# Performance work log

Measured on AMD Instinct MI355X. Metric: run time of the kernel, lower is better.

The kernel has to match this reference:

```python
import jax, jax.numpy as jnp
import numpy as np

L, S, R, NUM_RESNET = 6, 2, 3, 3
N = 2 ** L            # 64 blocks per axis
NX = N * S            # 128 grid points per axis
NCART_SIDE = 80
NCART = NCART_SIDE ** 2


def _perm_idx(L_, l):
    delta = 2 ** (L_ - l - 1)
    t = np.tile(np.arange(2) * delta, delta) + np.repeat(np.arange(delta), 2)
    t = np.tile(t, 2 ** l) + np.repeat(np.arange(2 ** l) * 2 ** (L_ - l), 2 ** (L_ - l))
    return jnp.asarray(t)


def _switch_idx(L_):
    h = L_ // 2
    t = np.tile(np.arange(2 ** h) * 2 ** h, 2 ** h) + np.repeat(np.arange(2 ** h), 2 ** h)
    return jnp.asarray(t)


def _bmm2(x, g_left, g_right):
    # x: (B,p,i,q,j). Right block-diag GEMM on (q,j), then left block-diag GEMM on (p,i).
    y = jnp.einsum('bpiqj,qjk->bpiqk', x, g_right)
    return jnp.einsum('bpiqk,pio->bpoqk', y, g_left)


def _complex_layer(xr, xi, p):
    # p: stacked (r1,i1,r2,i2,r3,i3,r4,i4); complex-style cross products of the original.
    r1, i1, r2, i2, r3, i3, r4, i4 = p
    yr = _bmm2(xr, r1, r1) + _bmm2(xr, i1, i1) + _bmm2(xi, r2, i2) + _bmm2(xi, i2, r2)
    yi = _bmm2(xi, r3, r3) + _bmm2(xi, i3, i3) + _bmm2(xr, r4, i4) + _bmm2(xr, i4, r4)
    return yr, yi


def _u_layer(xr, xi, p):
    ur1, ui1, ur2, ui2, ur3, ui3, ur4, ui4 = p
    return (_bmm2(xr, ur1, ur1) + _bmm2(xr, ui2, ui2)
            + _bmm2(xi, ur3, ui3) + _bmm2(xi, ui4, ur4))


def _permute(yr, yi, idx):
    yr = jnp.take(jnp.take(yr, idx, axis=1), idx, axis=3)
    yi = jnp.take(jnp.take(yi, idx, axis=1), idx, axis=3)
    return yr, yi


def _merge(y):  # (B,N,R,N,R) -> (B,N/2,2R,N/2,2R)
    return y.reshape(y.shape[0], N // 2, 2 * R, N // 2, 2 * R)


def _split(y):  # inverse of _merge
    return y.reshape(y.shape[0], N, R, N, R)


def reference(x, Vp, Hp, Mp, Gp, Up, cart_mat, r_index):
    B = x.shape[0]
    xr = x[..., 0].reshape(B, N, S, N, S)
    xi = x[..., 1].reshape(B, N, S, N, S)
    yr, yi = _complex_layer(xr, xi, Vp)                       # (B,N,R,N,R)
    for li, l in enumerate(range(L - 1, L // 2 - 1, -1)):     # H stages (permute then merge-GEMM)
        yr, yi = _permute(yr, yi, _perm_idx(L, l))
        yr, yi = _complex_layer(_merge(yr), _merge(yi), Hp[li])
        yr, yi = _split(yr), _split(yi)
    yr, yi = _permute(yr, yi, _switch_idx(L))                 # middle switch shuffle
    for k in range(NUM_RESNET):                               # residual M blocks
        zr, zi = _complex_layer(yr, yi, Mp[k])
        yr, yi = yr + zr, yi + zi
    for li, l in enumerate(range(L // 2 - 1, -1, -1)):        # G stages (merge-GEMM then permute)
        yr, yi = _complex_layer(_merge(yr), _merge(yi), Gp[li])
        yr, yi = _split(yr), _split(yi)
        yr, yi = _permute(yr, yi, _perm_idx(L, l))
    y = _u_layer(yr, yi, Up).reshape(B, NX * NX)              # real output, (B,NX,NX) flattened
    y = jnp.take(y, r_index, axis=1)                          # polar reindexing
    out = y @ cart_mat.T                                      # polar -> cartesian interpolation
    return out.reshape(B, NCART_SIDE, NCART_SIDE)


def setup_inputs() -> dict:
    key = jax.random.key(0)
    ks = jax.random.split(key, 9)
    B = 128
    x = jax.random.normal(ks[0], (B, NX, NX, 2), dtype=jnp.float32)
    Vp = jax.random.normal(ks[1], (8, N, S, R), dtype=jnp.float32) * 0.35
    Hp = jax.random.normal(ks[2], (L // 2, 8, N // 2, 2 * R, 2 * R), dtype=jnp.float32) * 0.2
    Mp = jax.random.normal(ks[3], (NUM_RESNET, 8, N, R, R), dtype=jnp.float32) * 0.25
    Gp = jax.random.normal(ks[4], (L // 2, 8, N // 2, 2 * R, 2 * R), dtype=jnp.float32) * 0.2
    Up = jax.random.normal(ks[5], (8, N, R, S), dtype=jnp.float32) * 0.35
    cart_mat = jax.random.normal(ks[6], (NCART, NX * NX), dtype=jnp.float32) * 0.01
    r_index = jax.random.permutation(ks[7], NX * NX).astype(jnp.int32)
    return {"x": x, "Vp": Vp, "Hp": Hp, "Mp": Mp, "Gp": Gp, "Up": Up,
            "cart_mat": cart_mat, "r_index": r_index}
```

## Files before the change

### kernel.cpp

```cpp
#include <hip/hip_runtime.h>


typedef _Float16 f16;
typedef __attribute__((ext_vector_type(8))) short sx8;
typedef __attribute__((ext_vector_type(4))) float fx4;
typedef __attribute__((ext_vector_type(8))) unsigned short usx8;
typedef __attribute__((ext_vector_type(4))) unsigned short usx4;

__device__ __forceinline__ unsigned short f2bf(float f) {
  unsigned u = __builtin_bit_cast(unsigned, f);
  u = (u + 0x7FFFu + ((u >> 16) & 1u)) >> 16;
  return (unsigned short)u;
}
__device__ __forceinline__ float bf2f(unsigned short h) {
  return __builtin_bit_cast(float, ((unsigned)h) << 16);
}

template<int ID>
__device__ __forceinline__ int rp_apply(int k) {
  if constexpr (ID == 0) { return k; }
  else if constexpr (ID == 3) { return (k & 7) * 8 + (k >> 3); }
  else {
    constexpr int l = (ID == 1) ? 4 : (ID == 2) ? 3 : (ID == 4) ? 2 : (ID == 5) ? 1 : 0;
    constexpr int d = 1 << (5 - l);
    constexpr int m2 = 2 * d;
    int g = k / m2, r = k % m2;
    return g * m2 + (r & 1) * d + (r >> 1);
  }
}

__global__ __launch_bounds__(256) void k_transpose(const float* __restrict__ x,
                                                   f16* __restrict__ xtr,
                                                   f16* __restrict__ xti) {
  __shared__ float ls[2][32][129];
  const int t = threadIdx.x;
  const int u = blockIdx.x;
  const int v0 = blockIdx.y * 32;
  for (int it = 0; it < 32; ++it) {
    int b = it * 4 + (t >> 6);
    int r = t & 63;
    int v = r >> 1, ch = r & 1;
    ls[ch][v][b] = x[(((size_t)b * 128 + u) * 128 + (v0 + v)) * 2 + ch];
  }
  __syncthreads();
  for (int it = 0; it < 32; ++it) {
    int idx = it * 256 + t;
    int ch = idx >> 12;
    int v = (idx >> 7) & 31;
    int b = idx & 127;
    f16* dst = ch ? xti : xtr;
    dst[((size_t)(u * 128 + v0 + v)) * 128 + b] = (f16)ls[ch][v][b];
  }
}

__global__ __launch_bounds__(128, 1) void k_vh(const f16* __restrict__ xtr,
                                               const f16* __restrict__ xti,
                                               f16* __restrict__ yr,
                                               f16* __restrict__ yi,
                                               const float* __restrict__ vp,
                                               const float* __restrict__ hp) {
  const int b = threadIdx.x;
  const int P = blockIdx.x, Q = blockIdx.y;
  float Vr[36], Vi[36];

#pragma unroll
  for (int pp = 0; pp < 2; ++pp)
#pragma unroll
    for (int qq = 0; qq < 2; ++qq) {
      const int p = 2 * P + pp, q = 2 * Q + qq;
      float Xr[4], Xi[4];
#pragma unroll
      for (int i = 0; i < 2; ++i)
#pragma unroll
        for (int j = 0; j < 2; ++j) {
          size_t off = ((size_t)((4 * P + 2 * pp + i) * 128 + (4 * Q + 2 * qq + j))) * 128 + b;
          Xr[i * 2 + j] = (float)xtr[off];
          Xi[i * 2 + j] = (float)xti[off];
        }
      float Ar[9], Ai[9];
#pragma unroll
      for (int k = 0; k < 9; ++k) { Ar[k] = 0.f; Ai[k] = 0.f; }
      auto termV = [&](float* Y, const float* X, int lm, int rm) {
        const float* Lw = vp + ((size_t)lm * 64 + p) * 6;
        const float* Rw = vp + ((size_t)rm * 64 + q) * 6;
#pragma unroll
        for (int i = 0; i < 2; ++i) {
          float t0 = X[i*2+0] * Rw[0] + X[i*2+1] * Rw[3];
          float t1 = X[i*2+0] * Rw[1] + X[i*2+1] * Rw[4];
          float t2 = X[i*2+0] * Rw[2] + X[i*2+1] * Rw[5];
#pragma unroll
          for (int o = 0; o < 3; ++o) {
            float lv = Lw[i * 3 + o];
            Y[o*3+0] += lv * t0; Y[o*3+1] += lv * t1; Y[o*3+2] += lv * t2;
          }
        }
      };
      termV(Ar, Xr, 0, 0); termV(Ar, Xr, 1, 1); termV(Ai, Xr, 6, 7); termV(Ai, Xr, 7, 6);
      termV(Ar, Xi, 2, 3); termV(Ar, Xi, 3, 2); termV(Ai, Xi, 4, 4); termV(Ai, Xi, 5, 5);
#pragma unroll
      for (int o = 0; o < 3; ++o)
#pragma unroll
        for (int k = 0; k < 3; ++k) {
          Vr[(3 * pp + o) * 6 + 3 * qq + k] = Ar[o * 3 + k];
          Vi[(3 * pp + o) * 6 + 3 * qq + k] = Ai[o * 3 + k];
        }
    }

  float Yr[36], Yi[36];
#pragma unroll
  for (int k = 0; k < 36; ++k) { Yr[k] = 0.f; Yi[k] = 0.f; }
  auto termH = [&](float* Y, const float* X, int lm, int rm) {
    const float* Lw = hp + ((size_t)lm * 32 + P) * 36;
    const float* Rw = hp + ((size_t)rm * 32 + Q) * 36;
#pragma unroll
    for (int i = 0; i < 6; ++i) {
      float tk[6];
#pragma unroll
      for (int k = 0; k < 6; ++k) tk[k] = 0.f;
#pragma unroll
      for (int j = 0; j < 6; ++j) {
        float xv = X[i * 6 + j];
#pragma unroll
        for (int k = 0; k < 6; ++k) tk[k] += xv * Rw[j * 6 + k];
      }
#pragma unroll
      for (int o = 0; o < 6; ++o) {
        float lv = Lw[i * 6 + o];
#pragma unroll
        for (int k = 0; k < 6; ++k) Y[o * 6 + k] += lv * tk[k];
      }
    }
  };
  termH(Yr, Vr, 0, 0); termH(Yr, Vr, 1, 1); termH(Yi, Vr, 6, 7); termH(Yi, Vr, 7, 6);
  termH(Yr, Vi, 2, 3); termH(Yr, Vi, 3, 2); termH(Yi, Vi, 4, 4); termH(Yi, Vi, 5, 5);

#pragma unroll
  for (int I = 0; I < 6; ++I)
#pragma unroll
    for (int J = 0; J < 6; ++J) {
      size_t off = ((size_t)((P * 6 + I) * 192 + (Q * 6 + J))) * 128 + b;
      yr[off] = (f16)Yr[I * 6 + J];
      yi[off] = (f16)Yi[I * 6 + J];
    }
}

template<int PERM>
__global__ __launch_bounds__(128, 1) void k_hg(const f16* __restrict__ xr,
                                               const f16* __restrict__ xi,
                                               f16* __restrict__ yr,
                                               f16* __restrict__ yi,
                                               const float* __restrict__ wp) {
  const int b = threadIdx.x;
  const int P = blockIdx.x, Q = blockIdx.y;
  int rrow[6], rcol[6];
#pragma unroll
  for (int I = 0; I < 6; ++I) {
    rrow[I] = rp_apply<PERM>(2 * P + I / 3) * 3 + I % 3;
    rcol[I] = rp_apply<PERM>(2 * Q + I / 3) * 3 + I % 3;
  }
  float X[36], Yr[36], Yi[36];
#pragma unroll
  for (int k = 0; k < 36; ++k) { Yr[k] = 0.f; Yi[k] = 0.f; }

  auto loadX = [&](const f16* src) {
#pragma unroll
    for (int I = 0; I < 6; ++I)
#pragma unroll
      for (int J = 0; J < 6; ++J)
        X[I * 6 + J] = (float)src[((size_t)(rrow[I] * 192 + rcol[J])) * 128 + b];
  };
  auto term = [&](float* Y, int lm, int rm) {
    const float* Lw = wp + ((size_t)lm * 32 + P) * 36;
    const float* Rw = wp + ((size_t)rm * 32 + Q) * 36;
#pragma unroll
    for (int i = 0; i < 6; ++i) {
      float tk[6];
#pragma unroll
      for (int k = 0; k < 6; ++k) tk[k] = 0.f;
#pragma unroll
      for (int j = 0; j < 6; ++j) {
        float xv = X[i * 6 + j];
#pragma unroll
        for (int k = 0; k < 6; ++k) tk[k] += xv * Rw[j * 6 + k];
      }
#pragma unroll
      for (int o = 0; o < 6; ++o) {
        float lv = Lw[i * 6 + o];
#pragma unroll
        for (int k = 0; k < 6; ++k) Y[o * 6 + k] += lv * tk[k];
      }
    }
  };
  loadX(xr);
  term(Yr, 0, 0); term(Yr, 1, 1); term(Yi, 6, 7); term(Yi, 7, 6);
  loadX(xi);
  term(Yr, 2, 3); term(Yr, 3, 2); term(Yi, 4, 4); term(Yi, 5, 5);
#pragma unroll
  for (int I = 0; I < 6; ++I)
#pragma unroll
    for (int J = 0; J < 6; ++J) {
      size_t off = ((size_t)((P * 6 + I) * 192 + (Q * 6 + J))) * 128 + b;
      yr[off] = (f16)Yr[I * 6 + J];
      yi[off] = (f16)Yi[I * 6 + J];
    }
}

__global__ __launch_bounds__(128, 1) void k_mg(const f16* __restrict__ xr,
                                               const f16* __restrict__ xi,
                                               f16* __restrict__ yr,
                                               f16* __restrict__ yi,
                                               const float* __restrict__ mp,
                                               const float* __restrict__ gp) {
  const int b = threadIdx.x;
  const int P = blockIdx.x, Q = blockIdx.y;
  float Vr[36], Vi[36];

#pragma unroll
  for (int aa = 0; aa < 2; ++aa)
#pragma unroll
    for (int bb = 0; bb < 2; ++bb) {
      const int p = 2 * P + aa, q = 2 * Q + bb;
      const int prow = rp_apply<3>(p) * 3, pcol = rp_apply<3>(q) * 3;
      float Xr[9], Xi[9];
#pragma unroll
      for (int i = 0; i < 3; ++i)
#pragma unroll
        for (int j = 0; j < 3; ++j) {
          size_t off = ((size_t)((prow + i) * 192 + (pcol + j))) * 128 + b;
          Xr[i * 3 + j] = (float)xr[off];
          Xi[i * 3 + j] = (float)xi[off];
        }
#pragma unroll
      for (int lk = 0; lk < 3; ++lk) {
        const float* wp = mp + (size_t)lk * (8 * 64 * 9);
        float Yr9[9], Yi9[9];
#pragma unroll
        for (int k = 0; k < 9; ++k) { Yr9[k] = Xr[k]; Yi9[k] = Xi[k]; }
        auto termM = [&](float* Y, const float* X, int lm, int rm) {
          const float* Lw = wp + ((size_t)lm * 64 + p) * 9;
          const float* Rw = wp + ((size_t)rm * 64 + q) * 9;
#pragma unroll
          for (int i = 0; i < 3; ++i) {
            float t0 = X[i*3+0] * Rw[0] + X[i*3+1] * Rw[3] + X[i*3+2] * Rw[6];
            float t1 = X[i*3+0] * Rw[1] + X[i*3+1] * Rw[4] + X[i*3+2] * Rw[7];
            float t2 = X[i*3+0] * Rw[2] + X[i*3+1] * Rw[5] + X[i*3+2] * Rw[8];
#pragma unroll
            for (int o = 0; o < 3; ++o) {
              float lv = Lw[i * 3 + o];
              Y[o*3+0] += lv * t0; Y[o*3+1] += lv * t1; Y[o*3+2] += lv * t2;
            }
          }
        };
        termM(Yr9, Xr, 0, 0); termM(Yr9, Xr, 1, 1); termM(Yi9, Xr, 6, 7); termM(Yi9, Xr, 7, 6);
        termM(Yr9, Xi, 2, 3); termM(Yr9, Xi, 3, 2); termM(Yi9, Xi, 4, 4); termM(Yi9, Xi, 5, 5);
#pragma unroll
        for (int k = 0; k < 9; ++k) { Xr[k] = Yr9[k]; Xi[k] = Yi9[k]; }
      }
#pragma unroll
      for (int i = 0; i < 3; ++i)
#pragma unroll
        for (int j = 0; j < 3; ++j) {
          Vr[(3 * aa + i) * 6 + 3 * bb + j] = Xr[i * 3 + j];
          Vi[(3 * aa + i) * 6 + 3 * bb + j] = Xi[i * 3 + j];
        }
    }

  float Yr[36], Yi[36];
#pragma unroll
  for (int k = 0; k < 36; ++k) { Yr[k] = 0.f; Yi[k] = 0.f; }
  auto termH = [&](float* Y, const float* X, int lm, int rm) {
    const float* Lw = gp + ((size_t)lm * 32 + P) * 36;
    const float* Rw = gp + ((size_t)rm * 32 + Q) * 36;
#pragma unroll
    for (int i = 0; i < 6; ++i) {
      float tk[6];
#pragma unroll
      for (int k = 0; k < 6; ++k) tk[k] = 0.f;
#pragma unroll
      for (int j = 0; j < 6; ++j) {
        float xv = X[i * 6 + j];
#pragma unroll
        for (int k = 0; k < 6; ++k) tk[k] += xv * Rw[j * 6 + k];
      }
#pragma unroll
      for (int o = 0; o < 6; ++o) {
        float lv = Lw[i * 6 + o];
#pragma unroll
        for (int k = 0; k < 6; ++k) Y[o * 6 + k] += lv * tk[k];
      }
    }
  };
  termH(Yr, Vr, 0, 0); termH(Yr, Vr, 1, 1); termH(Yi, Vr, 6, 7); termH(Yi, Vr, 7, 6);
  termH(Yr, Vi, 2, 3); termH(Yr, Vi, 3, 2); termH(Yi, Vi, 4, 4); termH(Yi, Vi, 5, 5);

#pragma unroll
  for (int I = 0; I < 6; ++I)
#pragma unroll
    for (int J = 0; J < 6; ++J) {
      size_t off = ((size_t)((P * 6 + I) * 192 + (Q * 6 + J))) * 128 + b;
      yr[off] = (f16)Yr[I * 6 + J];
      yi[off] = (f16)Yi[I * 6 + J];
    }
}

__global__ __launch_bounds__(128, 1) void k_u(const f16* __restrict__ xr,
                                              const f16* __restrict__ xi,
                                              unsigned short* __restrict__ ut,
                                              const float* __restrict__ wp) {
  const int b = threadIdx.x;
  const int p = blockIdx.x, q = blockIdx.y;
  int rrow[3], rcol[3];
#pragma unroll
  for (int i = 0; i < 3; ++i) {
    rrow[i] = rp_apply<6>(p) * 3 + i;
    rcol[i] = rp_apply<6>(q) * 3 + i;
  }
  float X[9], Y[4] = {0.f, 0.f, 0.f, 0.f};
  auto loadX = [&](const f16* src) {
#pragma unroll
    for (int i = 0; i < 3; ++i)
#pragma unroll
      for (int j = 0; j < 3; ++j)
        X[i * 3 + j] = (float)src[((size_t)(rrow[i] * 192 + rcol[j])) * 128 + b];
  };
  auto term = [&](int lm, int rm) {
    const float* Lw = wp + ((size_t)lm * 64 + p) * 6;
    const float* Rw = wp + ((size_t)rm * 64 + q) * 6;
#pragma unroll
    for (int i = 0; i < 3; ++i) {
      float t0 = X[i*3+0] * Rw[0] + X[i*3+1] * Rw[2] + X[i*3+2] * Rw[4];
      float t1 = X[i*3+0] * Rw[1] + X[i*3+1] * Rw[3] + X[i*3+2] * Rw[5];
      Y[0] += Lw[i*2+0] * t0; Y[1] += Lw[i*2+0] * t1;
      Y[2] += Lw[i*2+1] * t0; Y[3] += Lw[i*2+1] * t1;
    }
  };
  loadX(xr); term(0, 0); term(3, 3);
  loadX(xi); term(4, 5); term(7, 6);
#pragma unroll
  for (int o = 0; o < 2; ++o)
#pragma unroll
    for (int k = 0; k < 2; ++k)
      ut[((size_t)((p * 2 + o) * 128 + (q * 2 + k))) * 128 + b] = f2bf(Y[o * 2 + k]);
}

__global__ __launch_bounds__(256) void k_gather(const unsigned short* __restrict__ ut,
                                                const int* __restrict__ r_index,
                                                unsigned short* __restrict__ yg) {
  __shared__ unsigned short ls[64][130];
  __shared__ int ridx[64];
  const int t = threadIdx.x;
  const int m0 = blockIdx.x * 64;
  if (t < 64) ridx[t] = r_index[m0 + t];
  __syncthreads();
  for (int it = 0; it < 32; ++it) {
    int idx = it * 256 + t;
    int ml = idx >> 7, b = idx & 127;
    ls[ml][b] = ut[(size_t)ridx[ml] * 128 + b];
  }
  __syncthreads();
  int b = t >> 1, half = t & 1;
#pragma unroll
  for (int c = 0; c < 4; ++c) {
    usx8 v;
#pragma unroll
    for (int e = 0; e < 8; ++e) v[e] = ls[half * 32 + c * 8 + e][b];
    *(usx8*)(yg + (size_t)b * 16384 + m0 + half * 32 + c * 8) = v;
  }
}

#define G2_KC 8
#define G2_STEPS 32
#define G2_PITCH 72

__global__ __launch_bounds__(256) void k_gemm2(const unsigned short* __restrict__ yg,
                                               const float* __restrict__ cart,
                                               unsigned short* __restrict__ partial) {
  __shared__ unsigned short As[2][128][G2_PITCH];
  __shared__ unsigned short Bs[2][64][G2_PITCH];
  const int t = threadIdx.x;
  const int lane = t & 63, w = t >> 6;
  const int kc = blockIdx.x;
  const int c0 = blockIdx.y * 64;
  const int k0 = kc * 2048;

  fx4 acc[2][4];
#pragma unroll
  for (int i = 0; i < 2; ++i)
#pragma unroll
    for (int j = 0; j < 4; ++j) acc[i][j] = (fx4)0.f;

  auto ldA = [&](int rep, int kpos) -> usx8 {
    int c = t + rep * 256;
    return *(const usx8*)(yg + (size_t)(c >> 3) * 16384 + kpos + (c & 7) * 8);
  };
  auto stA = [&](int buf, int rep, usx8 v) {
    int c = t + rep * 256;
    *(usx8*)(&As[buf][c >> 3][(c & 7) * 8]) = v;
  };
  auto ldB = [&](int rep, int kpos, fx4* f0, fx4* f1) {
    int c = t + rep * 256;
    const float* p = cart + (size_t)(c0 + (c >> 3)) * 16384 + kpos + (c & 7) * 8;
    *f0 = *(const fx4*)p;
    *f1 = *(const fx4*)(p + 4);
  };
  auto stB = [&](int buf, int rep, fx4 f0, fx4 f1) {
    int c = t + rep * 256;
    usx8 v;
    v[0]=f2bf(f0[0]); v[1]=f2bf(f0[1]); v[2]=f2bf(f0[2]); v[3]=f2bf(f0[3]);
    v[4]=f2bf(f1[0]); v[5]=f2bf(f1[1]); v[6]=f2bf(f1[2]); v[7]=f2bf(f1[3]);
    *(usx8*)(&Bs[buf][c >> 3][(c & 7) * 8]) = v;
  };

  {
    usx8 a0 = ldA(0, k0), a1 = ldA(1, k0), a2 = ldA(2, k0), a3 = ldA(3, k0);
    fx4 b00, b01, b10, b11;
    ldB(0, k0, &b00, &b01); ldB(1, k0, &b10, &b11);
    stA(0, 0, a0); stA(0, 1, a1); stA(0, 2, a2); stA(0, 3, a3);
    stB(0, 0, b00, b01); stB(0, 1, b10, b11);
  }
  __syncthreads();

  for (int s = 0; s < G2_STEPS; ++s) {
    const int cur = s & 1;
    usx8 av[4]; fx4 b00, b01, b10, b11;
    const bool pf = (s + 1 < G2_STEPS);
    if (pf) {
      int kpos = k0 + (s + 1) * 64;
      av[0] = ldA(0, kpos); av[1] = ldA(1, kpos);
      av[2] = ldA(2, kpos); av[3] = ldA(3, kpos);
      ldB(0, kpos, &b00, &b01); ldB(1, kpos, &b10, &b11);
    }
    sx8 af[2][2], bf[4][2];
#pragma unroll
    for (int mi = 0; mi < 2; ++mi)
#pragma unroll
      for (int kk = 0; kk < 2; ++kk)
        af[mi][kk] = *(const sx8*)(&As[cur][w * 32 + mi * 16 + (lane & 15)][kk * 32 + (lane >> 4) * 8]);
#pragma unroll
    for (int ni = 0; ni < 4; ++ni)
#pragma unroll
      for (int kk = 0; kk < 2; ++kk)
        bf[ni][kk] = *(const sx8*)(&Bs[cur][ni * 16 + (lane & 15)][kk * 32 + (lane >> 4) * 8]);
#pragma unroll
    for (int kk = 0; kk < 2; ++kk)
#pragma unroll
      for (int mi = 0; mi < 2; ++mi)
#pragma unroll
        for (int ni = 0; ni < 4; ++ni)
          acc[mi][ni] = __builtin_amdgcn_mfma_f32_16x16x32_bf16(af[mi][kk], bf[ni][kk], acc[mi][ni], 0, 0, 0);
    if (pf) {
      stA(cur ^ 1, 0, av[0]); stA(cur ^ 1, 1, av[1]);
      stA(cur ^ 1, 2, av[2]); stA(cur ^ 1, 3, av[3]);
      stB(cur ^ 1, 0, b00, b01); stB(cur ^ 1, 1, b10, b11);
    }
    __syncthreads();
  }

#pragma unroll
  for (int mi = 0; mi < 2; ++mi) {
    int brow = w * 32 + mi * 16 + (lane >> 4) * 4;
#pragma unroll
    for (int ni = 0; ni < 4; ++ni) {
      int cc = c0 + ni * 16 + (lane & 15);
#pragma unroll
      for (int r = 0; r < 4; ++r)
        partial[((size_t)kc * 128 + brow + r) * 6400 + cc] = f2bf(acc[mi][ni][r]);
    }
  }
}

__global__ __launch_bounds__(256) void k_reduce2(const unsigned short* __restrict__ partial,
                                                 float* __restrict__ out) {
  int i = blockIdx.x * 256 + threadIdx.x;
  fx4 s = (fx4)0.f;
#pragma unroll
  for (int kc = 0; kc < G2_KC; ++kc) {
    usx4 v = *(const usx4*)(partial + (size_t)kc * 819200 + (size_t)i * 4);
    s[0] += bf2f(v[0]); s[1] += bf2f(v[1]); s[2] += bf2f(v[2]); s[3] += bf2f(v[3]);
  }
  *(fx4*)(out + (size_t)i * 4) = s;
}

extern "C" void kernel_launch(void* const* d_in, const int* in_sizes, int n_in,
                              void* d_out, int out_size, void* d_ws, size_t ws_size,
                              hipStream_t stream) {
  const float* x    = (const float*)d_in[0];
  const float* Vp   = (const float*)d_in[1];
  const float* Hp   = (const float*)d_in[2];
  const float* Mp   = (const float*)d_in[3];
  const float* Gp   = (const float*)d_in[4];
  const float* Up   = (const float*)d_in[5];
  const float* cart = (const float*)d_in[6];
  const int*   ridx = (const int*)d_in[7];
  float* out = (float*)d_out;
  unsigned short* hb = (unsigned short*)d_ws;

  const size_t PSZ = 4718592;
  f16* P0r = (f16*)(hb);
  f16* P0i = (f16*)(hb + PSZ);
  f16* P1r = (f16*)(hb + 2 * PSZ);
  f16* P1i = (f16*)(hb + 3 * PSZ);
  f16* xtr = (f16*)(hb + 4 * PSZ);
  f16* xti = (f16*)(hb + 4 * PSZ + 2097152);
  unsigned short* ut = hb + 4 * PSZ;
  unsigned short* yg = hb + 4 * PSZ + 2097152;
  unsigned short* partial = hb;

  const size_t HSZ = 8 * 32 * 36;

  k_transpose<<<dim3(128, 4), 256, 0, stream>>>(x, xtr, xti);
  k_vh<<<dim3(32, 32), 128, 0, stream>>>(xtr, xti, P0r, P0i, Vp, Hp + 0 * HSZ);
  k_hg<1><<<dim3(32, 32), 128, 0, stream>>>(P0r, P0i, P1r, P1i, Hp + 1 * HSZ);
  k_hg<2><<<dim3(32, 32), 128, 0, stream>>>(P1r, P1i, P0r, P0i, Hp + 2 * HSZ);
  k_mg<<<dim3(32, 32), 128, 0, stream>>>(P0r, P0i, P1r, P1i, Mp, Gp + 0 * HSZ);
  k_hg<4><<<dim3(32, 32), 128, 0, stream>>>(P1r, P1i, P0r, P0i, Gp + 1 * HSZ);
  k_hg<5><<<dim3(32, 32), 128, 0, stream>>>(P0r, P0i, P1r, P1i, Gp + 2 * HSZ);
  k_u<<<dim3(64, 64), 128, 0, stream>>>(P1r, P1i, ut, Up);
  k_gather<<<dim3(256), 256, 0, stream>>>(ut, ridx, yg);
  k_gemm2<<<dim3(G2_KC, 100), 256, 0, stream>>>(yg, cart, partial);
  k_reduce2<<<dim3(800), 256, 0, stream>>>(partial, out);
  (void)in_sizes; (void)n_in; (void)out_size; (void)ws_size;
}
```

Measured before the change: 333.7 us.

## Split block-diagonal layer work across four waves per block via LDS

The V/H, H/G and M/G stage kernels move from 128 threads per block, where each thread computed all eight complex-product terms for its batch column, to 512 threads per block. Each of the four 128-thread groups computes two terms, or one of the four sub-blocks in the V and M stages. Partial sums are combined through shared memory, and the H/G kernels stage the permuted inputs into LDS with 16-byte vector loads. This is meant to raise occupancy and parallelism and to relieve register pressure from the large per-thread unrolled arrays, at the cost of extra barriers, LDS traffic and a redundant-free but more serialized reduction. k_u also gets a launch bound that permits two blocks per CU.

Result: faster. 300.1 us (-10.1%).

```diff
diff --git a/kernel.cpp b/kernel.cpp
--- a/kernel.cpp
+++ b/kernel.cpp
@@ -26,6 +26,81 @@
     constexpr int m2 = 2 * d;
     int g = k / m2, r = k % m2;
     return g * m2 + (r & 1) * d + (r >> 1);
+  }
+}
+
+__device__ __forceinline__ void term_decode(int t, int& lm, int& rm,
+                                            bool& useXi, bool& toYi) {
+  lm = (t < 2) ? t : (t < 4) ? (t + 4) : (t - 2);
+  rm = (t >= 2 && t <= 5) ? (lm ^ 1) : lm;
+  useXi = (t >= 4);
+  toYi = (t >> 1) & 1;
+}
+
+#define SMEM_BYTES 36864
+
+__device__ __forceinline__ void layer6(int g, int b, int P, int Q,
+                                       const float* __restrict__ wp,
+                                       const f16* ldsX, float* Y0, float* Y1,
+                                       f16* __restrict__ yr,
+                                       f16* __restrict__ yi) {
+  int lm0, rm0, lm1, rm1;
+  switch (g) {
+    case 0:  lm0 = 0; rm0 = 0; lm1 = 1; rm1 = 1; break;
+    case 1:  lm0 = 6; rm0 = 7; lm1 = 7; rm1 = 6; break;
+    case 2:  lm0 = 2; rm0 = 3; lm1 = 3; rm1 = 2; break;
+    default: lm0 = 4; rm0 = 4; lm1 = 5; rm1 = 5; break;
+  }
+  const int xbase = (g & 2) ? 36 : 0;
+  float X[36], Y[36];
+#pragma unroll
+  for (int k = 0; k < 36; ++k) X[k] = (float)ldsX[(xbase + k) * 128 + b];
+#pragma unroll
+  for (int k = 0; k < 36; ++k) Y[k] = 0.f;
+
+  for (int tt = 0; tt < 2; ++tt) {
+    const int lm = tt ? lm1 : lm0;
+    const int rm = tt ? rm1 : rm0;
+    const float* Lw = wp + ((size_t)lm * 32 + P) * 36;
+    const float* Rw = wp + ((size_t)rm * 32 + Q) * 36;
+#pragma unroll
+    for (int i = 0; i < 6; ++i) {
+      float tk[6] = {0.f, 0.f, 0.f, 0.f, 0.f, 0.f};
+#pragma unroll
+      for (int j = 0; j < 6; ++j) {
+        float xv = X[i * 6 + j];
+#pragma unroll
+        for (int k = 0; k < 6; ++k) tk[k] += xv * Rw[j * 6 + k];
+      }
+#pragma unroll
+      for (int o = 0; o < 6; ++o) {
+        float lv = Lw[i * 6 + o];
+#pragma unroll
+        for (int k = 0; k < 6; ++k) Y[o * 6 + k] += lv * tk[k];
+      }
+    }
+  }
+  __syncthreads();
+  if (g == 2) {
+#pragma unroll
+    for (int k = 0; k < 36; ++k) Y0[k * 128 + b] = Y[k];
+  } else if (g == 3) {
+#pragma unroll
+    for (int k = 0; k < 36; ++k) Y1[k * 128 + b] = Y[k];
+  }
+  __syncthreads();
+  if (g == 0) {
+#pragma unroll
+    for (int k = 0; k < 36; ++k) {
+      float v = Y[k] + Y0[k * 128 + b];
+      yr[((size_t)((P * 6 + k / 6) * 192 + Q * 6 + k % 6)) * 128 + b] = (f16)v;
+    }
+  } else if (g == 1) {
+#pragma unroll
+    for (int k = 0; k < 36; ++k) {
+      float v = Y[k] + Y1[k * 128 + b];
+      yi[((size_t)((P * 6 + k / 6) * 192 + Q * 6 + k % 6)) * 128 + b] = (f16)v;
+    }
   }
 }
 
@@ -53,257 +128,183 @@
   }
 }
 
-__global__ __launch_bounds__(128, 1) void k_vh(const f16* __restrict__ xtr,
+__global__ __launch_bounds__(512, 4) void k_vh(const f16* __restrict__ xtr,
                                                const f16* __restrict__ xti,
                                                f16* __restrict__ yr,
                                                f16* __restrict__ yi,
                                                const float* __restrict__ vp,
                                                const float* __restrict__ hp) {
-  const int b = threadIdx.x;
+  __shared__ __align__(16) char smem[SMEM_BYTES];
+  f16* ldsX = (f16*)smem;
+  float* Y0 = (float*)smem;
+  float* Y1 = (float*)(smem + 18432);
+  const int t = threadIdx.x;
   const int P = blockIdx.x, Q = blockIdx.y;
-  float Vr[36], Vi[36];
-
-#pragma unroll
-  for (int pp = 0; pp < 2; ++pp)
-#pragma unroll
-    for (int qq = 0; qq < 2; ++qq) {
-      const int p = 2 * P + pp, q = 2 * Q + qq;
-      float Xr[4], Xi[4];
-#pragma unroll
-      for (int i = 0; i < 2; ++i)
-#pragma unroll
-        for (int j = 0; j < 2; ++j) {
-          size_t off = ((size_t)((4 * P + 2 * pp + i) * 128 + (4 * Q + 2 * qq + j))) * 128 + b;
-          Xr[i * 2 + j] = (float)xtr[off];
-          Xi[i * 2 + j] = (float)xti[off];
+  const int g = __builtin_amdgcn_readfirstlane(t >> 7);
+  const int b = t & 127;
+
+  const int pp = g >> 1, qq = g & 1;
+  const int p = 2 * P + pp, q = 2 * Q + qq;
+  float Xr[4], Xi[4];
+#pragma unroll
+  for (int i = 0; i < 2; ++i)
+#pragma unroll
+    for (int j = 0; j < 2; ++j) {
+      size_t off = ((size_t)((4 * P + 2 * pp + i) * 128 + (4 * Q + 2 * qq + j))) * 128 + b;
+      Xr[i * 2 + j] = (float)xtr[off];
+      Xi[i * 2 + j] = (float)xti[off];
+    }
+  float Ar[9], Ai[9];
+#pragma unroll
+  for (int k = 0; k < 9; ++k) { Ar[k] = 0.f; Ai[k] = 0.f; }
+  for (int tt = 0; tt < 8; ++tt) {
+    int lm, rm; bool useXi, toYi;
+    term_decode(tt, lm, rm, useXi, toYi);
+    const float* Lw = vp + ((size_t)lm * 64 + p) * 6;
+    const float* Rw = vp + ((size_t)rm * 64 + q) * 6;
+#pragma unroll
+    for (int i = 0; i < 2; ++i) {
+      float x0, x1;
+      if (useXi) { x0 = Xi[i * 2 + 0]; x1 = Xi[i * 2 + 1]; }
+      else       { x0 = Xr[i * 2 + 0]; x1 = Xr[i * 2 + 1]; }
+      float t0 = x0 * Rw[0] + x1 * Rw[3];
+      float t1 = x0 * Rw[1] + x1 * Rw[4];
+      float t2 = x0 * Rw[2] + x1 * Rw[5];
+      if (toYi) {
+#pragma unroll
+        for (int o = 0; o < 3; ++o) {
+          float lv = Lw[i * 3 + o];
+          Ai[o*3+0] += lv * t0; Ai[o*3+1] += lv * t1; Ai[o*3+2] += lv * t2;
         }
-      float Ar[9], Ai[9];
-#pragma unroll
-      for (int k = 0; k < 9; ++k) { Ar[k] = 0.f; Ai[k] = 0.f; }
-      auto termV = [&](float* Y, const float* X, int lm, int rm) {
-        const float* Lw = vp + ((size_t)lm * 64 + p) * 6;
-        const float* Rw = vp + ((size_t)rm * 64 + q) * 6;
-#pragma unroll
-        for (int i = 0; i < 2; ++i) {
-          float t0 = X[i*2+0] * Rw[0] + X[i*2+1] * Rw[3];
-          float t1 = X[i*2+0] * Rw[1] + X[i*2+1] * Rw[4];
-          float t2 = X[i*2+0] * Rw[2] + X[i*2+1] * Rw[5];
-#pragma unroll
-          for (int o = 0; o < 3; ++o) {
-            float lv = Lw[i * 3 + o];
-            Y[o*3+0] += lv * t0; Y[o*3+1] += lv * t1; Y[o*3+2] += lv * t2;
-          }
+      } else {
+#pragma unroll
+        for (int o = 0; o < 3; ++o) {
+          float lv = Lw[i * 3 + o];
+          Ar[o*3+0] += lv * t0; Ar[o*3+1] += lv * t1; Ar[o*3+2] += lv * t2;
         }
-      };
-      termV(Ar, Xr, 0, 0); termV(Ar, Xr, 1, 1); termV(Ai, Xr, 6, 7); termV(Ai, Xr, 7, 6);
-      termV(Ar, Xi, 2, 3); termV(Ar, Xi, 3, 2); termV(Ai, Xi, 4, 4); termV(Ai, Xi, 5, 5);
-#pragma unroll
-      for (int o = 0; o < 3; ++o)
-#pragma unroll
-        for (int k = 0; k < 3; ++k) {
-          Vr[(3 * pp + o) * 6 + 3 * qq + k] = Ar[o * 3 + k];
-          Vi[(3 * pp + o) * 6 + 3 * qq + k] = Ai[o * 3 + k];
-        }
-    }
-
-  float Yr[36], Yi[36];
-#pragma unroll
-  for (int k = 0; k < 36; ++k) { Yr[k] = 0.f; Yi[k] = 0.f; }
-  auto termH = [&](float* Y, const float* X, int lm, int rm) {
-    const float* Lw = hp + ((size_t)lm * 32 + P) * 36;
-    const float* Rw = hp + ((size_t)rm * 32 + Q) * 36;
-#pragma unroll
-    for (int i = 0; i < 6; ++i) {
-      float tk[6];
-#pragma unroll
-      for (int k = 0; k < 6; ++k) tk[k] = 0.f;
-#pragma unroll
-      for (int j = 0; j < 6; ++j) {
-        float xv = X[i * 6 + j];
-#pragma unroll
-        for (int k = 0; k < 6; ++k) tk[k] += xv * Rw[j * 6 + k];
       }
-#pragma unroll
-      for (int o = 0; o < 6; ++o) {
-        float lv = Lw[i * 6 + o];
-#pragma unroll
-        for (int k = 0; k < 6; ++k) Y[o * 6 + k] += lv * tk[k];
-      }
-    }
-  };
-  termH(Yr, Vr, 0, 0); termH(Yr, Vr, 1, 1); termH(Yi, Vr, 6, 7); termH(Yi, Vr, 7, 6);
-  termH(Yr, Vi, 2, 3); termH(Yr, Vi, 3, 2); termH(Yi, Vi, 4, 4); termH(Yi, Vi, 5, 5);
-
-#pragma unroll
-  for (int I = 0; I < 6; ++I)
-#pragma unroll
-    for (int J = 0; J < 6; ++J) {
-      size_t off = ((size_t)((P * 6 + I) * 192 + (Q * 6 + J))) * 128 + b;
-      yr[off] = (f16)Yr[I * 6 + J];
-      yi[off] = (f16)Yi[I * 6 + J];
-    }
+    }
+  }
+#pragma unroll
+  for (int o = 0; o < 3; ++o)
+#pragma unroll
+    for (int k = 0; k < 3; ++k) {
+      int ch = (3 * pp + o) * 6 + (3 * qq + k);
+      ldsX[ch * 128 + b] = (f16)Ar[o * 3 + k];
+      ldsX[(36 + ch) * 128 + b] = (f16)Ai[o * 3 + k];
+    }
+  __syncthreads();
+  layer6(g, b, P, Q, hp, ldsX, Y0, Y1, yr, yi);
 }
 
 template<int PERM>
-__global__ __launch_bounds__(128, 1) void k_hg(const f16* __restrict__ xr,
+__global__ __launch_bounds__(512, 4) void k_hg(const f16* __restrict__ xr,
                                                const f16* __restrict__ xi,
                                                f16* __restrict__ yr,
                                                f16* __restrict__ yi,
                                                const float* __restrict__ wp) {
-  const int b = threadIdx.x;
+  __shared__ __align__(16) char smem[SMEM_BYTES];
+  f16* ldsX = (f16*)smem;
+  float* Y0 = (float*)smem;
+  float* Y1 = (float*)(smem + 18432);
+  const int t = threadIdx.x;
   const int P = blockIdx.x, Q = blockIdx.y;
-  int rrow[6], rcol[6];
-#pragma unroll
-  for (int I = 0; I < 6; ++I) {
-    rrow[I] = rp_apply<PERM>(2 * P + I / 3) * 3 + I % 3;
-    rcol[I] = rp_apply<PERM>(2 * Q + I / 3) * 3 + I % 3;
-  }
-  float X[36], Yr[36], Yi[36];
-#pragma unroll
-  for (int k = 0; k < 36; ++k) { Yr[k] = 0.f; Yi[k] = 0.f; }
-
-  auto loadX = [&](const f16* src) {
-#pragma unroll
-    for (int I = 0; I < 6; ++I)
-#pragma unroll
-      for (int J = 0; J < 6; ++J)
-        X[I * 6 + J] = (float)src[((size_t)(rrow[I] * 192 + rcol[J])) * 128 + b];
-  };
-  auto term = [&](float* Y, int lm, int rm) {
-    const float* Lw = wp + ((size_t)lm * 32 + P) * 36;
-    const float* Rw = wp + ((size_t)rm * 32 + Q) * 36;
-#pragma unroll
-    for (int i = 0; i < 6; ++i) {
-      float tk[6];
-#pragma unroll
-      for (int k = 0; k < 6; ++k) tk[k] = 0.f;
-#pragma unroll
-      for (int j = 0; j < 6; ++j) {
-        float xv = X[i * 6 + j];
-#pragma unroll
-        for (int k = 0; k < 6; ++k) tk[k] += xv * Rw[j * 6 + k];
-      }
-#pragma unroll
-      for (int o = 0; o < 6; ++o) {
-        float lv = Lw[i * 6 + o];
-#pragma unroll
-        for (int k = 0; k < 6; ++k) Y[o * 6 + k] += lv * tk[k];
-      }
-    }
-  };
-  loadX(xr);
-  term(Yr, 0, 0); term(Yr, 1, 1); term(Yi, 6, 7); term(Yi, 7, 6);
-  loadX(xi);
-  term(Yr, 2, 3); term(Yr, 3, 2); term(Yi, 4, 4); term(Yi, 5, 5);
-#pragma unroll
-  for (int I = 0; I < 6; ++I)
-#pragma unroll
-    for (int J = 0; J < 6; ++J) {
-      size_t off = ((size_t)((P * 6 + I) * 192 + (Q * 6 + J))) * 128 + b;
-      yr[off] = (f16)Yr[I * 6 + J];
-      yi[off] = (f16)Yi[I * 6 + J];
-    }
-}
-
-__global__ __launch_bounds__(128, 1) void k_mg(const f16* __restrict__ xr,
+
+  for (int r = 0; r < 3; ++r) {
+    int idx = t + r * 512;
+    if (idx < 1152) {
+      int c = idx >> 4, o8 = (idx & 15) * 8;
+      int cc = (c < 36) ? c : c - 36;
+      int I = cc / 6, J = cc % 6;
+      int grow = rp_apply<PERM>(2 * P + I / 3) * 3 + I % 3;
+      int gcol = rp_apply<PERM>(2 * Q + J / 3) * 3 + J % 3;
+      const f16* src = (c < 36) ? xr : xi;
+      usx8 v = *(const usx8*)(src + ((size_t)(grow * 192 + gcol)) * 128 + o8);
+      *(usx8*)(ldsX + c * 128 + o8) = v;
+    }
+  }
+  __syncthreads();
+  const int g = __builtin_amdgcn_readfirstlane(t >> 7);
+  const int b = t & 127;
+  layer6(g, b, P, Q, wp, ldsX, Y0, Y1, yr, yi);
+}
+
+__global__ __launch_bounds__(512, 4) void k_mg(const f16* __restrict__ xr,
                                                const f16* __restrict__ xi,
                                                f16* __restrict__ yr,
                                                f16* __restrict__ yi,
                                                const float* __restrict__ mp,
                                                const float* __restrict__ gp) {
-  const int b = threadIdx.x;
+  __shared__ __align__(16) char smem[SMEM_BYTES];
+  f16* ldsX = (f16*)smem;
+  float* Y0 = (float*)smem;
+  float* Y1 = (float*)(smem + 18432);
+  const int t = threadIdx.x;
   const int P = blockIdx.x, Q = blockIdx.y;
-  float Vr[36], Vi[36];
-
-#pragma unroll
-  for (int aa = 0; aa < 2; ++aa)
-#pragma unroll
-    for (int bb = 0; bb < 2; ++bb) {
-      const int p = 2 * P + aa, q = 2 * Q + bb;
-      const int prow = rp_apply<3>(p) * 3, pcol = rp_apply<3>(q) * 3;
-      float Xr[9], Xi[9];
-#pragma unroll
-      for (int i = 0; i < 3; ++i)
-#pragma unroll
-        for (int j = 0; j < 3; ++j) {
-          size_t off = ((size_t)((prow + i) * 192 + (pcol + j))) * 128 + b;
-          Xr[i * 3 + j] = (float)xr[off];
-          Xi[i * 3 + j] = (float)xi[off];
+  const int g = __builtin_amdgcn_readfirstlane(t >> 7);
+  const int b = t & 127;
+
+  const int aa = g >> 1, bb = g & 1;
+  const int p = 2 * P + aa, q = 2 * Q + bb;
+  const int prow = rp_apply<3>(p) * 3, pcol = rp_apply<3>(q) * 3;
+  float Xr[9], Xi[9];
+#pragma unroll
+  for (int i = 0; i < 3; ++i)
+#pragma unroll
+    for (int j = 0; j < 3; ++j) {
+      size_t off = ((size_t)((prow + i) * 192 + (pcol + j))) * 128 + b;
+      Xr[i * 3 + j] = (float)xr[off];
+      Xi[i * 3 + j] = (float)xi[off];
+    }
+  for (int lk = 0; lk < 3; ++lk) {
+    const float* wp = mp + (size_t)lk * (8 * 64 * 9);
+    float Yr9[9], Yi9[9];
+#pragma unroll
+    for (int k = 0; k < 9; ++k) { Yr9[k] = Xr[k]; Yi9[k] = Xi[k]; }
+    for (int tt = 0; tt < 8; ++tt) {
+      int lm, rm; bool useXi, toYi;
+      term_decode(tt, lm, rm, useXi, toYi);
+      const float* Lw = wp + ((size_t)lm * 64 + p) * 9;
+      const float* Rw = wp + ((size_t)rm * 64 + q) * 9;
+#pragma unroll
+      for (int i = 0; i < 3; ++i) {
+        float x0, x1, x2;
+        if (useXi) { x0 = Xi[i*3+0]; x1 = Xi[i*3+1]; x2 = Xi[i*3+2]; }
+        else       { x0 = Xr[i*3+0]; x1 = Xr[i*3+1]; x2 = Xr[i*3+2]; }
+        float t0 = x0 * Rw[0] + x1 * Rw[3] + x2 * Rw[6];
+        float t1 = x0 * Rw[1] + x1 * Rw[4] + x2 * Rw[7];
+        float t2 = x0 * Rw[2] + x1 * Rw[5] + x2 * Rw[8];
+        if (toYi) {
+#pragma unroll
+          for (int o = 0; o < 3; ++o) {
+            float lv = Lw[i * 3 + o];
+            Yi9[o*3+0] += lv * t0; Yi9[o*3+1] += lv * t1; Yi9[o*3+2] += lv * t2;
+          }
+        } else {
+#pragma unroll
+          for (int o = 0; o < 3; ++o) {
+            float lv = Lw[i * 3 + o];
+            Yr9[o*3+0] += lv * t0; Yr9[o*3+1] += lv * t1; Yr9[o*3+2] += lv * t2;
+          }
         }
-#pragma unroll
-      for (int lk = 0; lk < 3; ++lk) {
-        const float* wp = mp + (size_t)lk * (8 * 64 * 9);
-        float Yr9[9], Yi9[9];
-#pragma unroll
-        for (int k = 0; k < 9; ++k) { Yr9[k] = Xr[k]; Yi9[k] = Xi[k]; }
-        auto termM = [&](float* Y, const float* X, int lm, int rm) {
-          const float* Lw = wp + ((size_t)lm * 64 + p) * 9;
-          const float* Rw = wp + ((size_t)rm * 64 + q) * 9;
-#pragma unroll
-          for (int i = 0; i < 3; ++i) {
-            float t0 = X[i*3+0] * Rw[0] + X[i*3+1] * Rw[3] + X[i*3+2] * Rw[6];
-            float t1 = X[i*3+0] * Rw[1] + X[i*3+1] * Rw[4] + X[i*3+2] * Rw[7];
-            float t2 = X[i*3+0] * Rw[2] + X[i*3+1] * Rw[5] + X[i*3+2] * Rw[8];
-#pragma unroll
-            for (int o = 0; o < 3; ++o) {
-              float lv = Lw[i * 3 + o];
-              Y[o*3+0] += lv * t0; Y[o*3+1] += lv * t1; Y[o*3+2] += lv * t2;
-            }
-          }
-        };
-        termM(Yr9, Xr, 0, 0); termM(Yr9, Xr, 1, 1); termM(Yi9, Xr, 6, 7); termM(Yi9, Xr, 7, 6);
-        termM(Yr9, Xi, 2, 3); termM(Yr9, Xi, 3, 2); termM(Yi9, Xi, 4, 4); termM(Yi9, Xi, 5, 5);
-#pragma unroll
-        for (int k = 0; k < 9; ++k) { Xr[k] = Yr9[k]; Xi[k] = Yi9[k]; }
       }
-#pragma unroll
-      for (int i = 0; i < 3; ++i)
-#pragma unroll
-        for (int j = 0; j < 3; ++j) {
-          Vr[(3 * aa + i) * 6 + 3 * bb + j] = Xr[i * 3 + j];
-          Vi[(3 * aa + i) * 6 + 3 * bb + j] = Xi[i * 3 + j];
-        }
-    }
-
-  float Yr[36], Yi[36];
-#pragma unroll
-  for (int k = 0; k < 36; ++k) { Yr[k] = 0.f; Yi[k] = 0.f; }
-  auto termH = [&](float* Y, const float* X, int lm, int rm) {
-    const float* Lw = gp + ((size_t)lm * 32 + P) * 36;
-    const float* Rw = gp + ((size_t)rm * 32 + Q) * 36;
-#pragma unroll
-    for (int i = 0; i < 6; ++i) {
-      float tk[6];
-#pragma unroll
-      for (int k = 0; k < 6; ++k) tk[k] = 0.f;
-#pragma unroll
-      for (int j = 0; j < 6; ++j) {
-        float xv = X[i * 6 + j];
-#pragma unroll
-        for (int k = 0; k < 6; ++k) tk[k] += xv * Rw[j * 6 + k];
-      }
-#pragma unroll
-      for (int o = 0; o < 6; ++o) {
-        float lv = Lw[i * 6 + o];
-#pragma unroll
-        for (int k = 0; k < 6; ++k) Y[o * 6 + k] += lv * tk[k];
-      }
-    }
-  };
-  termH(Yr, Vr, 0, 0); termH(Yr, Vr, 1, 1); termH(Yi, Vr, 6, 7); termH(Yi, Vr, 7, 6);
-  termH(Yr, Vi, 2, 3); termH(Yr, Vi, 3, 2); termH(Yi, Vi, 4, 4); termH(Yi, Vi, 5, 5);
-
-#pragma unroll
-  for (int I = 0; I < 6; ++I)
-#pragma unroll
-    for (int J = 0; J < 6; ++J) {
-      size_t off = ((size_t)((P * 6 + I) * 192 + (Q * 6 + J))) * 128 + b;
-      yr[off] = (f16)Yr[I * 6 + J];
-      yi[off] = (f16)Yi[I * 6 + J];
-    }
-}
-
-__global__ __launch_bounds__(128, 1) void k_u(const f16* __restrict__ xr,
+    }
+#pragma unroll
+    for (int k = 0; k < 9; ++k) { Xr[k] = Yr9[k]; Xi[k] = Yi9[k]; }
+  }
+#pragma unroll
+  for (int i = 0; i < 3; ++i)
+#pragma unroll
+    for (int j = 0; j < 3; ++j) {
+      int ch = (3 * aa + i) * 6 + (3 * bb + j);
+      ldsX[ch * 128 + b] = (f16)Xr[i * 3 + j];
+      ldsX[(36 + ch) * 128 + b] = (f16)Xi[i * 3 + j];
+    }
+  __syncthreads();
+  layer6(g, b, P, Q, gp, ldsX, Y0, Y1, yr, yi);
+}
+
+__global__ __launch_bounds__(128, 2) void k_u(const f16* __restrict__ xr,
                                               const f16* __restrict__ xi,
                                               unsigned short* __restrict__ ut,
                                               const float* __restrict__ wp) {
@@ -509,12 +510,12 @@
   const size_t HSZ = 8 * 32 * 36;
 
   k_transpose<<<dim3(128, 4), 256, 0, stream>>>(x, xtr, xti);
-  k_vh<<<dim3(32, 32), 128, 0, stream>>>(xtr, xti, P0r, P0i, Vp, Hp + 0 * HSZ);
-  k_hg<1><<<dim3(32, 32), 128, 0, stream>>>(P0r, P0i, P1r, P1i, Hp + 1 * HSZ);
-  k_hg<2><<<dim3(32, 32), 128, 0, stream>>>(P1r, P1i, P0r, P0i, Hp + 2 * HSZ);
-  k_mg<<<dim3(32, 32), 128, 0, stream>>>(P0r, P0i, P1r, P1i, Mp, Gp + 0 * HSZ);
-  k_hg<4><<<dim3(32, 32), 128, 0, stream>>>(P1r, P1i, P0r, P0i, Gp + 1 * HSZ);
-  k_hg<5><<<dim3(32, 32), 128, 0, stream>>>(P0r, P0i, P1r, P1i, Gp + 2 * HSZ);
+  k_vh<<<dim3(32, 32), 512, 0, stream>>>(xtr, xti, P0r, P0i, Vp, Hp + 0 * HSZ);
+  k_hg<1><<<dim3(32, 32), 512, 0, stream>>>(P0r, P0i, P1r, P1i, Hp + 1 * HSZ);
+  k_hg<2><<<dim3(32, 32), 512, 0, stream>>>(P1r, P1i, P0r, P0i, Hp + 2 * HSZ);
+  k_mg<<<dim3(32, 32), 512, 0, stream>>>(P0r, P0i, P1r, P1i, Mp, Gp + 0 * HSZ);
+  k_hg<4><<<dim3(32, 32), 512, 0, stream>>>(P1r, P1i, P0r, P0i, Gp + 1 * HSZ);
+  k_hg<5><<<dim3(32, 32), 512, 0, stream>>>(P0r, P0i, P1r, P1i, Gp + 2 * HSZ);
   k_u<<<dim3(64, 64), 128, 0, stream>>>(P1r, P1i, ut, Up);
   k_gather<<<dim3(256), 256, 0, stream>>>(ut, ridx, yg);
   k_gemm2<<<dim3(G2_KC, 100), 256, 0, stream>>>(yg, cart, partial);
```
